# Kernel tuning notes

Hardware: AMD Instinct MI355X
Metric: run time of the kernel (lower is better)

The kernel has to match this reference:

```python
import jax, jax.numpy as jnp
import numpy as np

B, S, D, H, FF, R, NB = 8, 1024, 768, 12, 3072, 16, 768


def _ln(x, g, b, eps=1e-6):
    m = x.mean(-1, keepdims=True)
    v = jnp.mean((x - m) ** 2, axis=-1, keepdims=True)
    return (x - m) * jax.lax.rsqrt(v + eps) * g + b


def setup_inputs() -> dict:
    key = jax.random.key(0)

    def rn(i, shape, s=0.02):
        return jax.random.normal(jax.random.fold_in(key, i), shape, jnp.float32) * s

    inp = {
        "x": jax.random.normal(jax.random.fold_in(key, 0), (B, S, D), jnp.float32),
        "attn_mask": jnp.zeros((S, S), jnp.float32),
        "norm1_g": jnp.ones((D,), jnp.float32),
        "norm1_b": jnp.zeros((D,), jnp.float32),
        "q_w": rn(1, (D, D)), "q_b": jnp.zeros((D,), jnp.float32),
        "k_w": rn(2, (D, D)), "k_b": jnp.zeros((D,), jnp.float32),
        "v_w": rn(3, (D, D)), "v_b": jnp.zeros((D,), jnp.float32),
        "o_w": rn(4, (D, D)), "o_b": jnp.zeros((D,), jnp.float32),
        "norm2_g": jnp.ones((D,), jnp.float32),
        "norm2_b": jnp.zeros((D,), jnp.float32),
        "fc1_w": rn(5, (FF, D)), "fc1_b": jnp.zeros((FF,), jnp.float32),
        "fc2_w": rn(6, (D, FF)), "fc2_b": jnp.zeros((D,), jnp.float32),
        # shared LoRA (backbone tokens)
        "lora1_A": rn(7, (D, R)), "lora1_B": rn(8, (R, FF)),
        "lora2_A": rn(9, (FF, R)), "lora2_B": rn(10, (R, D)),
        # expert VeRA: frozen shared A/B, per-expert diagonal scaling vectors
        "vera1_A": rn(11, (D, R)), "vera1_B": rn(12, (R, FF)),
        "vera2_A": rn(13, (FF, R)), "vera2_B": rn(14, (R, D)),
        "expert_fc1_d": rn(15, (R,), 1.0), "expert_fc1_b": rn(16, (FF,), 1.0),
        "expert_fc2_d": rn(17, (R,), 1.0), "expert_fc2_b": rn(18, (D,), 1.0),
        "num_backbone_tokens": NB,
    }
    return inp


def reference(x, attn_mask, norm1_g, norm1_b, q_w, q_b, k_w, k_b, v_w, v_b,
              o_w, o_b, norm2_g, norm2_b, fc1_w, fc1_b, fc2_w, fc2_b,
              lora1_A, lora1_B, lora2_A, lora2_B,
              vera1_A, vera1_B, vera2_A, vera2_B,
              expert_fc1_d, expert_fc1_b, expert_fc2_d, expert_fc2_b,
              num_backbone_tokens):
    bsz, seq, dim = x.shape
    hd = dim // H                      # head_dim = 64
    scale = hd ** -0.5
    nb = num_backbone_tokens

    # ---- attention (manual bmm + mask + softmax, eval-mode dropout = identity) ----
    h = _ln(x, norm1_g, norm1_b)
    q = (h @ q_w.T + q_b).reshape(bsz, seq, H, hd)
    k = (h @ k_w.T + k_b).reshape(bsz, seq, H, hd)
    v = (h @ v_w.T + v_b).reshape(bsz, seq, H, hd)
    scores = jnp.einsum('bqhd,bkhd->bhqk', q * scale, k) + attn_mask  # [B,H,S,S]
    probs = jax.nn.softmax(scores, axis=-1)
    ao = jnp.einsum('bhqk,bkhd->bqhd', probs, v).reshape(bsz, seq, dim)
    x = x + (ao @ o_w.T + o_b)

    # ---- MLP with split backbone (shared LoRA) / expert (VeRA) adapters ----
    residual = x
    n2 = _ln(x, norm2_g, norm2_b)
    hid = n2 @ fc1_w.T + fc1_b                                   # [B,S,FF]
    hid_b = hid[:, :nb] + (n2[:, :nb] @ lora1_A) @ lora1_B
    hid_e = hid[:, nb:] + (((n2[:, nb:] @ vera1_A) * expert_fc1_d) @ vera1_B) * expert_fc1_b
    hid = jnp.concatenate([hid_b, hid_e], axis=1)
    hid = jax.nn.gelu(hid)
    out = hid @ fc2_w.T + fc2_b                                  # [B,S,D]
    out_b = out[:, :nb] + (hid[:, :nb] @ lora2_A) @ lora2_B
    out_e = out[:, nb:] + (((hid[:, nb:] @ vera2_A) * expert_fc2_d) @ vera2_B) * expert_fc2_b
    out = jnp.concatenate([out_b, out_e], axis=1)
    return residual + out
```

## Files before the change

kernel.cpp:

```cpp
#include <hip/hip_runtime.h>
#include <stdint.h>

#define B_  8
#define S_  1024
#define D_  768
#define H_  12
#define HD_ 64
#define FF_ 3072
#define M_  (B_*S_)
#define R_  16
#define QLD 2304
#define KBLK 128

typedef unsigned short u16;
typedef short s16x8 __attribute__((ext_vector_type(8)));
typedef float fx4  __attribute__((ext_vector_type(4)));

__device__ __forceinline__ float b2f(u16 u) {
  union { unsigned int i; float f; } c; c.i = ((unsigned int)u) << 16; return c.f;
}
__device__ __forceinline__ u16 f2b(float f) {
  union { float f; unsigned int i; } c; c.f = f;
  unsigned int x = c.i;
  x += 0x7FFFu + ((x >> 16) & 1u);
  return (u16)(x >> 16);
}
__device__ __forceinline__ float gelu_f(float x) {
  float u = 0.7978845608028654f * (x + 0.044715f * x * x * x);
  float e = __expf(2.f * u);
  float t = 1.f - 2.f / (e + 1.f);
  return 0.5f * x * (1.f + t);
}
__device__ __forceinline__ void gload16(const u16* gsrc, u16* ldst) {
  __builtin_amdgcn_global_load_lds(
      (__attribute__((address_space(1))) void*)(gsrc),
      (__attribute__((address_space(3))) void*)(ldst), 16, 0, 0);
}

__global__ __launch_bounds__(256)
void cvt_prep(const float* __restrict__ q_w, const float* __restrict__ k_w,
              const float* __restrict__ v_w, const float* __restrict__ o_w,
              const float* __restrict__ fc1_w, const float* __restrict__ fc2_w,
              u16* __restrict__ wqkv, u16* __restrict__ wo,
              u16* __restrict__ wfc1, u16* __restrict__ wfc2,
              const float* __restrict__ q_bv, const float* __restrict__ k_bv,
              const float* __restrict__ v_bv, float* __restrict__ qkvb,
              const float* __restrict__ lora1B, const float* __restrict__ vera1B,
              const float* __restrict__ e1b, u16* __restrict__ up1L, u16* __restrict__ up1V,
              const float* __restrict__ lora2B, const float* __restrict__ vera2B,
              const float* __restrict__ e2b, u16* __restrict__ up2L, u16* __restrict__ up2V,
              const float* __restrict__ lora2A, const float* __restrict__ vera2A,
              u16* __restrict__ a2tL, u16* __restrict__ a2tV)
{
  const int i = blockIdx.x * 256 + threadIdx.x;
  const int q1  = D_ * D_ / 4;
  const int fd4 = FF_ * D_ / 4;
  {
    const float* s; u16* d; int j;
    if      (i <     q1)       { s = q_w;   d = wqkv;            j = i; }
    else if (i < 2 * q1)       { s = k_w;   d = wqkv + D_*D_;    j = i - q1; }
    else if (i < 3 * q1)       { s = v_w;   d = wqkv + 2*D_*D_;  j = i - 2*q1; }
    else if (i < 4 * q1)       { s = o_w;   d = wo;              j = i - 3*q1; }
    else if (i < 4 * q1 + fd4) { s = fc1_w; d = wfc1;            j = i - 4*q1; }
    else                       { s = fc2_w; d = wfc2;            j = i - 4*q1 - fd4; }
    const float4 f = ((const float4*)s)[j];
    ushort4 o4; o4.x = f2b(f.x); o4.y = f2b(f.y); o4.z = f2b(f.z); o4.w = f2b(f.w);
    ((ushort4*)d)[j] = o4;
  }
  if (i < FF_) {
    const int f = i;
    if (f < QLD)
      qkvb[f] = (f < D_) ? q_bv[f] : (f < 2 * D_) ? k_bv[f - D_] : v_bv[f - 2 * D_];
    {
      const float ev = e1b[f];
      #pragma unroll
      for (int r = 0; r < 16; ++r) {
        up1L[(size_t)f * 32 + r] = f2b(lora1B[(size_t)r * FF_ + f]);
        up1V[(size_t)f * 32 + r] = f2b(vera1B[(size_t)r * FF_ + f] * ev);
        up1L[(size_t)f * 32 + 16 + r] = 0;
        up1V[(size_t)f * 32 + 16 + r] = 0;
      }
    }
    {
      const float4* apl = (const float4*)(lora2A + (size_t)f * 16);
      const float4* apv = (const float4*)(vera2A + (size_t)f * 16);
      #pragma unroll
      for (int q4 = 0; q4 < 4; ++q4) {
        const float4 l4 = apl[q4], v4 = apv[q4];
        a2tL[(size_t)(q4*4+0) * FF_ + f] = f2b(l4.x);
        a2tL[(size_t)(q4*4+1) * FF_ + f] = f2b(l4.y);
        a2tL[(size_t)(q4*4+2) * FF_ + f] = f2b(l4.z);
        a2tL[(size_t)(q4*4+3) * FF_ + f] = f2b(l4.w);
        a2tV[(size_t)(q4*4+0) * FF_ + f] = f2b(v4.x);
        a2tV[(size_t)(q4*4+1) * FF_ + f] = f2b(v4.y);
        a2tV[(size_t)(q4*4+2) * FF_ + f] = f2b(v4.z);
        a2tV[(size_t)(q4*4+3) * FF_ + f] = f2b(v4.w);
      }
    }
    if (f < D_) {
      const float ev = e2b[f];
      #pragma unroll
      for (int r = 0; r < 16; ++r) {
        up2L[(size_t)f * 32 + r] = f2b(lora2B[(size_t)r * D_ + f]);
        up2V[(size_t)f * 32 + r] = f2b(vera2B[(size_t)r * D_ + f] * ev);
        up2L[(size_t)f * 32 + 16 + r] = 0;
        up2V[(size_t)f * 32 + 16 + r] = 0;
      }
    }
  }
}

template<bool ADD>
__global__ __launch_bounds__(256)
void ln_k(const float* __restrict__ x, const u16* __restrict__ add,
          const float* __restrict__ g, const float* __restrict__ beta,
          u16* __restrict__ outb, float* __restrict__ xsum,
          const float* __restrict__ Alora, const float* __restrict__ Avera,
          const float* __restrict__ dvec, u16* __restrict__ tmp1b,
          const int* __restrict__ nbp)
{
  const int row = blockIdx.x;
  const size_t base = (size_t)row * D_;
  float v0[3]; float s = 0.f, sq = 0.f;
  #pragma unroll
  for (int i = 0; i < 3; ++i) {
    const int d = threadIdx.x + i * 256;
    float val = x[base + d];
    if (ADD) { val += b2f(add[base + d]); xsum[base + d] = val; }
    v0[i] = val; s += val; sq += val * val;
  }
  #pragma unroll
  for (int mm = 32; mm >= 1; mm >>= 1) { s += __shfl_xor(s, mm); sq += __shfl_xor(sq, mm); }
  __shared__ float ss[4], s2[4];
  if ((threadIdx.x & 63) == 0) { ss[threadIdx.x >> 6] = s; s2[threadIdx.x >> 6] = sq; }
  __syncthreads();
  s  = ss[0] + ss[1] + ss[2] + ss[3];
  sq = s2[0] + s2[1] + s2[2] + s2[3];
  const float mean = s * (1.f / D_);
  const float var  = sq * (1.f / D_) - mean * mean;
  const float rs   = rsqrtf(var + 1e-6f);
  float nv[3];
  #pragma unroll
  for (int i = 0; i < 3; ++i) {
    const int d = threadIdx.x + i * 256;
    nv[i] = (v0[i] - mean) * rs * g[d] + beta[d];
    outb[base + d] = f2b(nv[i]);
  }

  if (ADD) {
    const int nb = *nbp;
    const bool ex = (row % S_) >= nb;
    const float* Am = ex ? Avera : Alora;
    float p[16];
    #pragma unroll
    for (int r = 0; r < 16; ++r) p[r] = 0.f;
    #pragma unroll
    for (int i = 0; i < 3; ++i) {
      const int d = threadIdx.x + i * 256;
      const float4* ap = (const float4*)(Am + (size_t)d * R_);
      const float4 a0 = ap[0], a1 = ap[1], a2 = ap[2], a3 = ap[3];
      const float vv = nv[i];
      p[0]  += vv * a0.x; p[1]  += vv * a0.y; p[2]  += vv * a0.z; p[3]  += vv * a0.w;
      p[4]  += vv * a1.x; p[5]  += vv * a1.y; p[6]  += vv * a1.z; p[7]  += vv * a1.w;
      p[8]  += vv * a2.x; p[9]  += vv * a2.y; p[10] += vv * a2.z; p[11] += vv * a2.w;
      p[12] += vv * a3.x; p[13] += vv * a3.y; p[14] += vv * a3.z; p[15] += vv * a3.w;
    }
    #pragma unroll
    for (int st = 1; st < 16; st <<= 1)
      #pragma unroll
      for (int r = 0; r < 16; ++r) p[r] += __shfl_xor(p[r], st);
    __shared__ float sred[16][16];
    const int grp = threadIdx.x >> 4;
    if ((threadIdx.x & 15) == 0) {
      #pragma unroll
      for (int r = 0; r < 16; ++r) sred[grp][r] = p[r];
    }
    __syncthreads();
    if (threadIdx.x < 16) {
      float v = 0.f;
      #pragma unroll
      for (int gg = 0; gg < 16; ++gg) v += sred[gg][threadIdx.x];
      if (ex) v *= dvec[threadIdx.x];
      tmp1b[(size_t)row * 32 + threadIdx.x] = f2b(v);
      tmp1b[(size_t)row * 32 + 16 + threadIdx.x] = 0;
    }
  }
}

template<int MODE>
__global__ __launch_bounds__(256)
void gemm_bt(const u16* __restrict__ A, const u16* __restrict__ W,
             const float* __restrict__ bias, u16* __restrict__ Cb,
             float* __restrict__ Cf, const float* __restrict__ resid,
             const u16* __restrict__ Aad, const u16* __restrict__ BadL,
             const u16* __restrict__ BadV, const int* __restrict__ nbp,
             int M, int N, int K)
{
  __shared__ u16 As[2][128 * 32];
  __shared__ u16 Bs[2][128 * 32];
  const int tid   = threadIdx.x;
  const int lane  = tid & 63;
  const int wid   = tid >> 6;
  const int wr    = wid >> 1;
  const int wc    = wid & 1;
  const int lr    = lane & 15;
  const int lk    = (lane >> 4) << 3;
  const int gn    = N >> 7;
  const int nwg   = (M >> 7) * gn;
  const int chunk = nwg >> 3;
  const int lin   = blockIdx.x;
  const int swz   = (lin & 7) * chunk + (lin >> 3);
  const int m0    = (swz / gn) * 128;
  const int n0    = (swz % gn) * 128;
  const int kg    = (tid & 3) * 8;
  const int row_a = tid >> 2;

  const int nst = K >> 5;
  const int tot = (MODE >= 1) ? nst + 1 : nst;
  const u16* Bad = nullptr;
  if (MODE >= 1) Bad = ((m0 % S_) >= *nbp) ? BadV : BadL;

  const u16* arow = A + (size_t)(m0 + row_a) * K + kg;
  const u16* wrow = W + (size_t)(n0 + row_a) * K + kg;
  const size_t half_a = (size_t)64 * K;

  fx4 acc[4][4];
  const fx4 zero = {0.f, 0.f, 0.f, 0.f};
  #pragma unroll
  for (int i = 0; i < 4; ++i)
    #pragma unroll
    for (int j = 0; j < 4; ++j) acc[i][j] = zero;

  gload16(arow,          &As[0][tid * 8]);
  gload16(arow + half_a, &As[0][(256 + tid) * 8]);
  gload16(wrow,          &Bs[0][tid * 8]);
  gload16(wrow + half_a, &Bs[0][(256 + tid) * 8]);
  __syncthreads();

  for (int t = 0; t < tot; ++t) {
    const int cur = t & 1;
    if (t + 1 < tot) {
      const int nxt = cur ^ 1;
      if (MODE >= 1 && t + 1 == nst) {
        gload16(Aad + (size_t)(m0 + row_a) * 32 + kg,      &As[nxt][tid * 8]);
        gload16(Aad + (size_t)(m0 + 64 + row_a) * 32 + kg, &As[nxt][(256 + tid) * 8]);
        gload16(Bad + (size_t)(n0 + row_a) * 32 + kg,      &Bs[nxt][tid * 8]);
        gload16(Bad + (size_t)(n0 + 64 + row_a) * 32 + kg, &Bs[nxt][(256 + tid) * 8]);
      } else {
        const size_t ko = (size_t)(t + 1) * 32;
        gload16(arow + ko,          &As[nxt][tid * 8]);
        gload16(arow + ko + half_a, &As[nxt][(256 + tid) * 8]);
        gload16(wrow + ko,          &Bs[nxt][tid * 8]);
        gload16(wrow + ko + half_a, &Bs[nxt][(256 + tid) * 8]);
      }
    }
    s16x8 av[4], bv[4];
    #pragma unroll
    for (int i = 0; i < 4; ++i)
      av[i] = *(const s16x8*)&As[cur][(wr * 64 + i * 16 + lr) * 32 + lk];
    #pragma unroll
    for (int j = 0; j < 4; ++j)
      bv[j] = *(const s16x8*)&Bs[cur][(wc * 64 + j * 16 + lr) * 32 + lk];
    __builtin_amdgcn_s_setprio(1);
    #pragma unroll
    for (int i = 0; i < 4; ++i)
      #pragma unroll
      for (int j = 0; j < 4; ++j)
        acc[i][j] = __builtin_amdgcn_mfma_f32_16x16x32_bf16(av[i], bv[j], acc[i][j], 0, 0, 0);
    __builtin_amdgcn_s_setprio(0);
    __syncthreads();
  }

  const int rb = (lane >> 4) * 4;
  #pragma unroll
  for (int j = 0; j < 4; ++j) {
    const int col = n0 + wc * 64 + j * 16 + lr;
    const float bj = bias ? bias[col] : 0.f;
    #pragma unroll
    for (int i = 0; i < 4; ++i) {
      const int row = m0 + wr * 64 + i * 16 + rb;
      #pragma unroll
      for (int r = 0; r < 4; ++r) {
        const float val = acc[i][j][r] + bj;
        const size_t idx = (size_t)(row + r) * N + col;
        if (MODE == 1)      Cb[idx] = f2b(gelu_f(val));
        else if (MODE == 2) Cf[idx] = resid[idx] + val;
        else                Cb[idx] = f2b(val);
      }
    }
  }
}

__global__ __launch_bounds__(256)
void downproj(const u16* __restrict__ hid, const u16* __restrict__ A2tL,
              const u16* __restrict__ A2tV, float* __restrict__ part,
              const int* __restrict__ nbp)
{
  __shared__ u16 As[2][128 * 32];
  __shared__ u16 Bs[2][16 * 32];
  const int tid  = threadIdx.x;
  const int lane = tid & 63;
  const int w    = tid >> 6;
  const int lr   = lane & 15;
  const int lk   = (lane >> 4) << 3;
  const int m0   = blockIdx.x * 128;
  const int kb   = blockIdx.y * (FF_ / 8);
  const int nb   = *nbp;
  const u16* A2t = ((m0 % S_) >= nb) ? A2tV : A2tL;
  const int kg    = (tid & 3) * 8;
  const int row_a = tid >> 2;

  const u16* hrow = hid + (size_t)(m0 + row_a) * FF_ + kb + kg;
  const size_t half_h = (size_t)64 * FF_;
  const u16* brow = A2t + (size_t)(tid >> 2) * FF_ + kb + kg;

  const fx4 zero = {0.f, 0.f, 0.f, 0.f};
  fx4 acc[2]; acc[0] = zero; acc[1] = zero;

  const int nst = (FF_ / 8) >> 5;
  gload16(hrow,          &As[0][tid * 8]);
  gload16(hrow + half_h, &As[0][(256 + tid) * 8]);
  if (tid < 64) gload16(brow, &Bs[0][tid * 8]);
  __syncthreads();

  for (int t = 0; t < nst; ++t) {
    const int cur = t & 1;
    if (t + 1 < nst) {
      const int nxt = cur ^ 1;
      const size_t ko = (size_t)(t + 1) * 32;
      gload16(hrow + ko,          &As[nxt][tid * 8]);
      gload16(hrow + ko + half_h, &As[nxt][(256 + tid) * 8]);
      if (tid < 64) gload16(brow + ko, &Bs[nxt][tid * 8]);
    }
    s16x8 bv = *(const s16x8*)&Bs[cur][lr * 32 + lk];
    #pragma unroll
    for (int i = 0; i < 2; ++i) {
      s16x8 av = *(const s16x8*)&As[cur][(w * 32 + i * 16 + lr) * 32 + lk];
      acc[i] = __builtin_amdgcn_mfma_f32_16x16x32_bf16(av, bv, acc[i], 0, 0, 0);
    }
    __syncthreads();
  }

  const int rb = (lane >> 4) * 4;
  #pragma unroll
  for (int i = 0; i < 2; ++i)
    #pragma unroll
    for (int r = 0; r < 4; ++r)
      part[(size_t)blockIdx.y * M_ * 16 +
           (size_t)(m0 + w * 32 + i * 16 + rb + r) * 16 + lr] = acc[i][r];
}

__global__ __launch_bounds__(256)
void reduce_dp(const float* __restrict__ part, const float* __restrict__ d2,
               u16* __restrict__ tmp2b, const int* __restrict__ nbp)
{
  const int idx = blockIdx.x * 256 + threadIdx.x;
  const int m = idx >> 4, r = idx & 15;
  const int nb = *nbp;
  float s = 0.f;
  #pragma unroll
  for (int ks = 0; ks < 8; ++ks) s += part[(size_t)ks * M_ * 16 + idx];
  if ((m % S_) >= nb) s *= d2[r];
  tmp2b[(size_t)m * 32 + r] = f2b(s);
  tmp2b[(size_t)m * 32 + 16 + r] = 0;
}

__global__ __launch_bounds__(256)
void attn_mfma(const u16* __restrict__ qkv, const float* __restrict__ mask,
               u16* __restrict__ o)
{
  __shared__ u16 Kl[2][128 * 64];
  __shared__ u16 Vt[2][64 * 128];
  __shared__ uint32_t Pl[4][1024];

  const int tid  = threadIdx.x;
  const int lane = tid & 63;
  const int wq   = tid >> 6;
  const int lr   = lane & 15;
  const int hi   = lane >> 4;
  const int lin = blockIdx.x;
  const int vsw = (lin & 7) * 192 + (lin >> 3);
  const int qb  = vsw & 15;
  const int bh  = vsw >> 4;
  const int b    = bh / H_;
  const int h    = bh % H_;
  const size_t tok0 = (size_t)b * S_ + (size_t)qb * 64;
  const size_t colh = (size_t)h * HD_;

  const int va  = tid >> 3;
  const int vc8 = (tid & 7) * 8;
  u16* qstage = (u16*)&Pl[0][0];

  #pragma unroll
  for (int u = 0; u < 2; ++u) {
    const int li = u * 256 + tid;
    const int r  = li >> 3;
    const int cb = ((li & 7) ^ (r & 7)) * 8;
    gload16(qkv + (tok0 + r) * QLD + colh + cb, &qstage[li * 8]);
  }
  {
    const size_t ktok = (size_t)b * S_;
    #pragma unroll
    for (int u = 0; u < 4; ++u) {
      const int li = u * 256 + tid;
      const int r  = li >> 3;
      const int cb = ((li & 7) ^ (r & 7)) * 8;
      gload16(qkv + (ktok + r) * QLD + D_ + colh + cb, &Kl[0][li * 8]);
    }
    const u16* vp = qkv + (ktok + 4 * va) * QLD + 2 * D_ + colh + vc8;
    s16x8 w0 = *(const s16x8*)vp;
    s16x8 w1 = *(const s16x8*)(vp + QLD);
    s16x8 w2 = *(const s16x8*)(vp + 2 * QLD);
    s16x8 w3 = *(const s16x8*)(vp + 3 * QLD);
    #pragma unroll
    for (int jj = 0; jj < 8; ++jj) {
      const int d  = vc8 + jj;
      const int sw = ((d & 7) ^ ((d >> 3) & 7)) << 3;
      const int cp = (4 * va) ^ sw;
      *(uint32_t*)&Vt[0][d * 128 + cp] =
          (uint32_t)(u16)w0[jj] | ((uint32_t)(u16)w1[jj] << 16);
      *(uint32_t*)&Vt[0][d * 128 + cp + 2] =
          (uint32_t)(u16)w2[jj] | ((uint32_t)(u16)w3[jj] << 16);
    }
  }
  __syncthreads();

  s16x8 qa[2];
  {
    const int qrow = wq * 16 + lr;
    #pragma unroll
    for (int ks = 0; ks < 2; ++ks)
      qa[ks] = *(const s16x8*)&qstage[qrow * 64 + ((ks * 32 + hi * 8) ^ ((qrow & 7) << 3))];
  }
  __syncthreads();

  const fx4 zero = {0.f, 0.f, 0.f, 0.f};
  fx4 oacc[4];
  #pragma unroll
  for (int dj = 0; dj < 4; ++dj) oacc[dj] = zero;
  float mreg = -3.0e38f, lreg = 0.f;

  const int NT = S_ / KBLK;
  for (int kt = 0; kt < NT; ++kt) {
    const int cur = kt & 1;
    const int nxt = cur ^ 1;

    s16x8 w0, w1, w2, w3;
    if (kt + 1 < NT) {
      const size_t ktokn = (size_t)b * S_ + (size_t)(kt + 1) * KBLK;
      #pragma unroll
      for (int u = 0; u < 4; ++u) {
        const int li = u * 256 + tid;
        const int r  = li >> 3;
        const int cb = ((li & 7) ^ (r & 7)) * 8;
        gload16(qkv + (ktokn + r) * QLD + D_ + colh + cb, &Kl[nxt][li * 8]);
      }
      const u16* vp = qkv + (ktokn + 4 * va) * QLD + 2 * D_ + colh + vc8;
      w0 = *(const s16x8*)vp;
      w1 = *(const s16x8*)(vp + QLD);
      w2 = *(const s16x8*)(vp + 2 * QLD);
      w3 = *(const s16x8*)(vp + 3 * QLD);
    }

    float val[8][4];
    #pragma unroll
    for (int jh = 0; jh < 2; ++jh) {
      s16x8 kb2[4][2];
      #pragma unroll
      for (int j = 0; j < 4; ++j) {
        const int n = (jh * 4 + j) * 16 + lr;
        #pragma unroll
        for (int ks = 0; ks < 2; ++ks)
          kb2[j][ks] = *(const s16x8*)&Kl[cur][n * 64 + ((ks * 32 + hi * 8) ^ ((n & 7) << 3))];
      }
      fx4 m4[4];
      {
        const float* mp = mask + (size_t)(qb * 64 + wq * 16 + lr) * S_
                        + (size_t)kt * KBLK + jh * 64 + 4 * hi;
        #pragma unroll
        for (int j = 0; j < 4; ++j)
          m4[j] = *(const fx4*)(mp + j * 16);
      }
      fx4 sf[4];
      #pragma unroll
      for (int j = 0; j < 4; ++j) sf[j] = zero;
      __builtin_amdgcn_s_setprio(1);
      #pragma unroll
      for (int ks = 0; ks < 2; ++ks)
        #pragma unroll
        for (int j = 0; j < 4; ++j)
          sf[j] = __builtin_amdgcn_mfma_f32_16x16x32_bf16(kb2[j][ks], qa[ks], sf[j], 0, 0, 0);
      __builtin_amdgcn_s_setprio(0);
      #pragma unroll
      for (int j = 0; j < 4; ++j)
        #pragma unroll
        for (int r = 0; r < 4; ++r)
          val[jh * 4 + j][r] = sf[j][r] * 0.125f + m4[j][r];
    }

    {
      float mk[8];
      #pragma unroll
      for (int kg = 0; kg < 8; ++kg)
        mk[kg] = fmaxf(fmaxf(val[kg][0], val[kg][1]), fmaxf(val[kg][2], val[kg][3]));
      float mx = fmaxf(fmaxf(fmaxf(mk[0], mk[1]), fmaxf(mk[2], mk[3])),
                       fmaxf(fmaxf(mk[4], mk[5]), fmaxf(mk[6], mk[7])));
      mx = fmaxf(mx, __shfl_xor(mx, 16));
      mx = fmaxf(mx, __shfl_xor(mx, 32));
      const bool noresc = (bool)__all(mx <= mreg + 8.f);
      float fac = 1.f;
      if (!noresc) {
        const float mn = fmaxf(mreg, mx);
        fac = __expf(mreg - mn);
        mreg = mn;
      }
      float sk[8];
      #pragma unroll
      for (int kg = 0; kg < 8; ++kg) {
        #pragma unroll
        for (int r = 0; r < 4; ++r) val[kg][r] = __expf(val[kg][r] - mreg);
        sk[kg] = (val[kg][0] + val[kg][1]) + (val[kg][2] + val[kg][3]);
      }
      float rs = ((sk[0] + sk[1]) + (sk[2] + sk[3])) + ((sk[4] + sk[5]) + (sk[6] + sk[7]));
      rs += __shfl_xor(rs, 16);
      rs += __shfl_xor(rs, 32);
      lreg = lreg * fac + rs;
      if (!noresc) {
        float facr[4];
        #pragma unroll
        for (int r = 0; r < 4; ++r) facr[r] = __shfl(fac, hi * 4 + r);
        #pragma unroll
        for (int dj = 0; dj < 4; ++dj)
          #pragma unroll
          for (int r = 0; r < 4; ++r) oacc[dj][r] *= facr[r];
      }
    }

    {
      uint32_t* prow = &Pl[wq][lr * 64];
      #pragma unroll
      for (int kg = 0; kg < 8; ++kg) {
        const uint32_t p0 = __builtin_amdgcn_perm(
            __float_as_uint(val[kg][1]), __float_as_uint(val[kg][0]), 0x07060302u);
        const uint32_t p1 = __builtin_amdgcn_perm(
            __float_as_uint(val[kg][3]), __float_as_uint(val[kg][2]), 0x07060302u);
        const int i0 = (8 * kg + 2 * hi) ^ ((lr & 7) << 3);
        uint2 pk; pk.x = p0; pk.y = p1;
        *(uint2*)&prow[i0] = pk;
      }
    }

    if (kt + 1 < NT) {
      #pragma unroll
      for (int jj = 0; jj < 8; ++jj) {
        const int d  = vc8 + jj;
        const int sw = ((d & 7) ^ ((d >> 3) & 7)) << 3;
        const int cp = (4 * va) ^ sw;
        *(uint32_t*)&Vt[nxt][d * 128 + cp] =
            (uint32_t)(u16)w0[jj] | ((uint32_t)(u16)w1[jj] << 16);
        *(uint32_t*)&Vt[nxt][d * 128 + cp + 2] =
            (uint32_t)(u16)w2[jj] | ((uint32_t)(u16)w3[jj] << 16);
      }
    }

    #pragma unroll
    for (int ks = 0; ks < 4; ++ks) {
      const int pbase = (16 * ks + 4 * hi) ^ ((lr & 7) << 3);
      s16x8 pa = *(const s16x8*)&Pl[wq][lr * 64 + pbase];
      s16x8 bv2[4];
      #pragma unroll
      for (int dj = 0; dj < 4; ++dj) {
        const int n  = dj * 16 + lr;
        const int sw = ((n & 7) ^ ((n >> 3) & 7)) << 3;
        bv2[dj] = *(const s16x8*)&Vt[cur][n * 128 + ((ks * 32 + hi * 8) ^ sw)];
      }
      __builtin_amdgcn_s_setprio(1);
      #pragma unroll
      for (int dj = 0; dj < 4; ++dj)
        oacc[dj] = __builtin_amdgcn_mfma_f32_16x16x32_bf16(pa, bv2[dj], oacc[dj], 0, 0, 0);
      __builtin_amdgcn_s_setprio(0);
    }

    __syncthreads();
  }

  {
    const float linv = 1.f / lreg;
    float invr[4];
    #pragma unroll
    for (int r = 0; r < 4; ++r) invr[r] = __shfl(linv, hi * 4 + r);
    #pragma unroll
    for (int r = 0; r < 4; ++r) {
      const size_t grow = (tok0 + wq * 16 + hi * 4 + r) * D_ + colh;
      #pragma unroll
      for (int dj = 0; dj < 4; ++dj)
        o[grow + dj * 16 + lr] = f2b(oacc[dj][r] * invr[r]);
    }
  }
}

extern "C" void kernel_launch(void* const* d_in, const int* in_sizes, int n_in,
                              void* d_out, int out_size, void* d_ws, size_t ws_size,
                              hipStream_t stream)
{
  const float* x      = (const float*)d_in[0];
  const float* mask   = (const float*)d_in[1];
  const float* n1g    = (const float*)d_in[2];
  const float* n1b    = (const float*)d_in[3];
  const float* q_w    = (const float*)d_in[4];
  const float* q_bv   = (const float*)d_in[5];
  const float* k_w    = (const float*)d_in[6];
  const float* k_bv   = (const float*)d_in[7];
  const float* v_w    = (const float*)d_in[8];
  const float* v_bv   = (const float*)d_in[9];
  const float* o_w    = (const float*)d_in[10];
  const float* o_bv   = (const float*)d_in[11];
  const float* n2g    = (const float*)d_in[12];
  const float* n2b    = (const float*)d_in[13];
  const float* fc1_w  = (const float*)d_in[14];
  const float* fc1_bv = (const float*)d_in[15];
  const float* fc2_w  = (const float*)d_in[16];
  const float* fc2_bv = (const float*)d_in[17];
  const float* lora1A = (const float*)d_in[18];
  const float* lora1B = (const float*)d_in[19];
  const float* lora2A = (const float*)d_in[20];
  const float* lora2B = (const float*)d_in[21];
  const float* vera1A = (const float*)d_in[22];
  const float* vera1B = (const float*)d_in[23];
  const float* vera2A = (const float*)d_in[24];
  const float* vera2B = (const float*)d_in[25];
  const float* e1d    = (const float*)d_in[26];
  const float* e1b    = (const float*)d_in[27];
  const float* e2d    = (const float*)d_in[28];
  const float* e2b    = (const float*)d_in[29];
  const int*   nbp    = (const int*)d_in[30];

  char* wsb = (char*)d_ws;
  u16* h1    = (u16*)wsb; wsb += (size_t)M_ * D_ * 2;
  u16* qkv   = (u16*)wsb; wsb += (size_t)M_ * QLD * 2;
  u16* attno = (u16*)wsb; wsb += (size_t)M_ * D_ * 2;
  u16* oproj = (u16*)wsb; wsb += (size_t)M_ * D_ * 2;
  u16* n2    = (u16*)wsb; wsb += (size_t)M_ * D_ * 2;
  u16* wqkv  = (u16*)wsb; wsb += (size_t)QLD * D_ * 2;
  u16* wo    = (u16*)wsb; wsb += (size_t)D_ * D_ * 2;
  u16* wfc1  = (u16*)wsb; wsb += (size_t)FF_ * D_ * 2;
  u16* wfc2  = (u16*)wsb; wsb += (size_t)D_ * FF_ * 2;
  u16* tmp1b = (u16*)wsb; wsb += (size_t)M_ * 32 * 2;
  u16* tmp2b = (u16*)wsb; wsb += (size_t)M_ * 32 * 2;
  u16* up1L  = (u16*)wsb; wsb += (size_t)FF_ * 32 * 2;
  u16* up1V  = (u16*)wsb; wsb += (size_t)FF_ * 32 * 2;
  u16* up2L  = (u16*)wsb; wsb += (size_t)D_ * 32 * 2;
  u16* up2V  = (u16*)wsb; wsb += (size_t)D_ * 32 * 2;
  u16* a2tL  = (u16*)wsb; wsb += (size_t)16 * FF_ * 2;
  u16* a2tV  = (u16*)wsb; wsb += (size_t)16 * FF_ * 2;
  float* qkvb = (float*)wsb; wsb += (size_t)QLD * 4;
  float* part = (float*)wsb; wsb += (size_t)8 * M_ * 16 * 4;
  u16* hidb = h1;

  const int totq = (4 * D_ * D_ + 2 * FF_ * D_) / 4;
  cvt_prep<<<totq / 256, 256, 0, stream>>>(q_w, k_w, v_w, o_w, fc1_w, fc2_w,
                                           wqkv, wo, wfc1, wfc2,
                                           q_bv, k_bv, v_bv, qkvb,
                                           lora1B, vera1B, e1b, up1L, up1V,
                                           lora2B, vera2B, e2b, up2L, up2V,
                                           lora2A, vera2A, a2tL, a2tV);

  ln_k<false><<<M_, 256, 0, stream>>>(x, nullptr, n1g, n1b, h1, nullptr,
                                      nullptr, nullptr, nullptr, nullptr, nullptr);
  gemm_bt<0><<<(M_/128) * (QLD/128), 256, 0, stream>>>(
      h1, wqkv, qkvb, qkv, nullptr, nullptr, nullptr, nullptr, nullptr, nullptr,
      M_, QLD, D_);
  attn_mfma<<<(S_/64) * (B_*H_), 256, 0, stream>>>(qkv, mask, attno);
  gemm_bt<0><<<(M_/128) * (D_/128), 256, 0, stream>>>(
      attno, wo, o_bv, oproj, nullptr, nullptr, nullptr, nullptr, nullptr, nullptr,
      M_, D_, D_);

  ln_k<true><<<M_, 256, 0, stream>>>(x, oproj, n2g, n2b, n2, (float*)d_out,
                                     lora1A, vera1A, e1d, tmp1b, nbp);

  gemm_bt<1><<<(M_/128) * (FF_/128), 256, 0, stream>>>(
      n2, wfc1, fc1_bv, hidb, nullptr, nullptr, tmp1b, up1L, up1V, nbp,
      M_, FF_, D_);

  downproj<<<dim3(M_/128, 8), 256, 0, stream>>>(hidb, a2tL, a2tV, part, nbp);
  reduce_dp<<<M_*16/256, 256, 0, stream>>>(part, e2d, tmp2b, nbp);

  gemm_bt<2><<<(M_/128) * (D_/128), 256, 0, stream>>>(
      hidb, wfc2, fc2_bv, nullptr, (float*)d_out, (const float*)d_out,
      tmp2b, up2L, up2V, nbp, M_, D_, FF_);
}
```

Measured before the change: 364.8 us.

## Double K-tile depth in GEMM with XOR-swizzled LDS and explicit barriers

The bf16 GEMM now stages 64-wide K tiles instead of 32, which halves the number of loop iterations and barriers and gives each LDS fetch two MFMA k-steps. The shared-memory layout uses an XOR swizzle on 16-byte chunks so that row-strided fragment reads avoid bank conflicts. The low-rank adapter tail is loaded during the last iteration and processed in a separate epilogue step. Synchronisation switches to explicit waitcnt, s_barrier and sched_barrier calls. In exchange, LDS use doubles to 64KB per block, which may lower occupancy.

```diff
diff --git a/kernel.cpp b/kernel.cpp
--- a/kernel.cpp
+++ b/kernel.cpp
@@ -196,15 +196,15 @@
              const u16* __restrict__ BadV, const int* __restrict__ nbp,
              int M, int N, int K)
 {
-  __shared__ u16 As[2][128 * 32];
-  __shared__ u16 Bs[2][128 * 32];
+  __shared__ u16 As[2][128 * 64];
+  __shared__ u16 Bs[2][128 * 64];
   const int tid   = threadIdx.x;
   const int lane  = tid & 63;
   const int wid   = tid >> 6;
   const int wr    = wid >> 1;
   const int wc    = wid & 1;
   const int lr    = lane & 15;
-  const int lk    = (lane >> 4) << 3;
+  const int hi    = lane >> 4;
   const int gn    = N >> 7;
   const int nwg   = (M >> 7) * gn;
   const int chunk = nwg >> 3;
@@ -212,17 +212,15 @@
   const int swz   = (lin & 7) * chunk + (lin >> 3);
   const int m0    = (swz / gn) * 128;
   const int n0    = (swz % gn) * 128;
-  const int kg    = (tid & 3) * 8;
-  const int row_a = tid >> 2;
-
-  const int nst = K >> 5;
-  const int tot = (MODE >= 1) ? nst + 1 : nst;
+
+  const int nst = K >> 6;
   const u16* Bad = nullptr;
   if (MODE >= 1) Bad = ((m0 % S_) >= *nbp) ? BadV : BadL;
 
-  const u16* arow = A + (size_t)(m0 + row_a) * K + kg;
-  const u16* wrow = W + (size_t)(n0 + row_a) * K + kg;
-  const size_t half_a = (size_t)64 * K;
+  const int sr[4]  = { tid >> 3, (256 + tid) >> 3, (512 + tid) >> 3, (768 + tid) >> 3 };
+  int scb[4];
+  #pragma unroll
+  for (int u = 0; u < 4; ++u) scb[u] = (((u * 256 + tid) & 7) ^ (sr[u] & 7)) * 8;
 
   fx4 acc[4][4];
   const fx4 zero = {0.f, 0.f, 0.f, 0.f};
@@ -231,47 +229,87 @@
     #pragma unroll
     for (int j = 0; j < 4; ++j) acc[i][j] = zero;
 
-  gload16(arow,          &As[0][tid * 8]);
-  gload16(arow + half_a, &As[0][(256 + tid) * 8]);
-  gload16(wrow,          &Bs[0][tid * 8]);
-  gload16(wrow + half_a, &Bs[0][(256 + tid) * 8]);
+  #pragma unroll
+  for (int u = 0; u < 4; ++u) {
+    gload16(A + (size_t)(m0 + sr[u]) * K + scb[u], &As[0][(u * 256 + tid) * 8]);
+    gload16(W + (size_t)(n0 + sr[u]) * K + scb[u], &Bs[0][(u * 256 + tid) * 8]);
+  }
   __syncthreads();
 
-  for (int t = 0; t < tot; ++t) {
-    const int cur = t & 1;
-    if (t + 1 < tot) {
-      const int nxt = cur ^ 1;
-      if (MODE >= 1 && t + 1 == nst) {
-        gload16(Aad + (size_t)(m0 + row_a) * 32 + kg,      &As[nxt][tid * 8]);
-        gload16(Aad + (size_t)(m0 + 64 + row_a) * 32 + kg, &As[nxt][(256 + tid) * 8]);
-        gload16(Bad + (size_t)(n0 + row_a) * 32 + kg,      &Bs[nxt][tid * 8]);
-        gload16(Bad + (size_t)(n0 + 64 + row_a) * 32 + kg, &Bs[nxt][(256 + tid) * 8]);
-      } else {
-        const size_t ko = (size_t)(t + 1) * 32;
-        gload16(arow + ko,          &As[nxt][tid * 8]);
-        gload16(arow + ko + half_a, &As[nxt][(256 + tid) * 8]);
-        gload16(wrow + ko,          &Bs[nxt][tid * 8]);
-        gload16(wrow + ko + half_a, &Bs[nxt][(256 + tid) * 8]);
-      }
-    }
-    s16x8 av[4], bv[4];
+  for (int kt = 0; kt < nst; ++kt) {
+    const int c = kt & 1;
+    const bool more = (kt + 1 < nst);
+    if (more) {
+      const int ko = (kt + 1) << 6;
+      #pragma unroll
+      for (int u = 0; u < 4; ++u) {
+        gload16(A + (size_t)(m0 + sr[u]) * K + ko + scb[u], &As[c ^ 1][(u * 256 + tid) * 8]);
+        gload16(W + (size_t)(n0 + sr[u]) * K + ko + scb[u], &Bs[c ^ 1][(u * 256 + tid) * 8]);
+      }
+    } else if (MODE >= 1) {
+      #pragma unroll
+      for (int u = 0; u < 2; ++u) {
+        const int li = u * 256 + tid;
+        const int r  = li >> 2;
+        const int cg = (li & 3) * 8;
+        gload16(Aad + (size_t)(m0 + r) * 32 + cg, &As[c ^ 1][li * 8]);
+        gload16(Bad + (size_t)(n0 + r) * 32 + cg, &Bs[c ^ 1][li * 8]);
+      }
+    }
+    __builtin_amdgcn_sched_barrier(0);
+
+    s16x8 av[4][2], bv[4][2];
+    #pragma unroll
+    for (int i = 0; i < 4; ++i) {
+      const int row = wr * 64 + i * 16 + lr;
+      const int rb7 = row & 7;
+      #pragma unroll
+      for (int ks = 0; ks < 2; ++ks)
+        av[i][ks] = *(const s16x8*)&As[c][row * 64 + (((ks * 4 + hi) ^ rb7) * 8)];
+    }
+    #pragma unroll
+    for (int j = 0; j < 4; ++j) {
+      const int row = wc * 64 + j * 16 + lr;
+      const int rb7 = row & 7;
+      #pragma unroll
+      for (int ks = 0; ks < 2; ++ks)
+        bv[j][ks] = *(const s16x8*)&Bs[c][row * 64 + (((ks * 4 + hi) ^ rb7) * 8)];
+    }
+    __builtin_amdgcn_s_setprio(1);
+    #pragma unroll
+    for (int ks = 0; ks < 2; ++ks)
+      #pragma unroll
+      for (int i = 0; i < 4; ++i)
+        #pragma unroll
+        for (int j = 0; j < 4; ++j)
+          acc[i][j] = __builtin_amdgcn_mfma_f32_16x16x32_bf16(av[i][ks], bv[j][ks], acc[i][j], 0, 0, 0);
+    __builtin_amdgcn_s_setprio(0);
+
+    if (more || MODE >= 1) {
+      __builtin_amdgcn_sched_barrier(0);
+      asm volatile("s_waitcnt vmcnt(0) lgkmcnt(0)" ::: "memory");
+      __builtin_amdgcn_s_barrier();
+      __builtin_amdgcn_sched_barrier(0);
+    }
+  }
+
+  if (MODE >= 1) {
+    const int ad = nst & 1;
+    s16x8 aav[4], abv[4];
     #pragma unroll
     for (int i = 0; i < 4; ++i)
-      av[i] = *(const s16x8*)&As[cur][(wr * 64 + i * 16 + lr) * 32 + lk];
+      aav[i] = *(const s16x8*)&As[ad][(wr * 64 + i * 16 + lr) * 32 + hi * 8];
     #pragma unroll
     for (int j = 0; j < 4; ++j)
-      bv[j] = *(const s16x8*)&Bs[cur][(wc * 64 + j * 16 + lr) * 32 + lk];
-    __builtin_amdgcn_s_setprio(1);
+      abv[j] = *(const s16x8*)&Bs[ad][(wc * 64 + j * 16 + lr) * 32 + hi * 8];
     #pragma unroll
     for (int i = 0; i < 4; ++i)
       #pragma unroll
       for (int j = 0; j < 4; ++j)
-        acc[i][j] = __builtin_amdgcn_mfma_f32_16x16x32_bf16(av[i], bv[j], acc[i][j], 0, 0, 0);
-    __builtin_amdgcn_s_setprio(0);
-    __syncthreads();
-  }
-
-  const int rb = (lane >> 4) * 4;
+        acc[i][j] = __builtin_amdgcn_mfma_f32_16x16x32_bf16(aav[i], abv[j], acc[i][j], 0, 0, 0);
+  }
+
+  const int rb = hi * 4;
   #pragma unroll
   for (int j = 0; j < 4; ++j) {
     const int col = n0 + wc * 64 + j * 16 + lr;
```

Result: faster. 347.7 us (-4.7%).
